# Optimization experiments

Measured on AMD Instinct MI355X. Metric: run time of the kernel, lower is better.

## Reference

```python
import jax, jax.numpy as jnp
import numpy as np

N, D_IN, D_HID, D_OUT, E = 8192, 1024, 4096, 1024, 8
N_ACTIVE = max(1, int(E * 0.625))  # 5
TEMP = float(np.e)               # temperature = np.e in source


def setup_inputs() -> dict:
    key = jax.random.key(0)
    ks = jax.random.split(key, 4)
    return {
        "x": jax.random.normal(ks[0], (N, D_IN), jnp.float32),
        "gate_w": jax.random.normal(ks[1], (D_IN, E), jnp.float32) * 0.02,
        "gate_b": jnp.zeros((E,), jnp.float32),
        "w1": jax.random.normal(ks[2], (E, D_IN, D_HID), jnp.float32) * 0.02,
        "b1": jnp.zeros((E, D_HID), jnp.float32),
        "w2": jax.random.normal(ks[3], (E, D_HID, D_OUT), jnp.float32) * 0.02,
        "b2": jnp.zeros((E, D_OUT), jnp.float32),
    }


def reference(x, gate_w, gate_b, w1, b1, w2, b2):
    # Gate: softmax over experts at temperature e, then top-k mask + renormalize
    scores = (x @ gate_w + gate_b) / TEMP                 # [N, E]
    probs = jax.nn.softmax(scores, axis=-1)               # [N, E]
    _, topk_idx = jax.lax.top_k(probs, N_ACTIVE)          # [N, k]
    mask = jax.nn.one_hot(topk_idx, E, dtype=probs.dtype).sum(axis=-2)  # [N, E]
    weights = probs * mask
    weights = weights / (weights.sum(axis=-1, keepdims=True) + 1e-8)
    # Dense all-experts FFN (dropout is eval-mode identity)
    h = jax.nn.relu(jnp.einsum('nd,edh->neh', x, w1) + b1)   # [N, E, d_hid]
    e_out = jnp.einsum('neh,eho->neo', h, w2) + b2           # [N, E, d_out]
    # Camp A (first E/2 experts) added, camp G subtracted: out = out_a - out_g
    sign = jnp.where(jnp.arange(E) < E // 2, 1.0, -1.0)      # [E]
    return jnp.einsum('ne,neo->no', weights * sign, e_out)   # [N, d_out]
```

## Files before the change

kernel.cpp:

```cpp
#include <hip/hip_runtime.h>
#include <hip/hip_bf16.h>
#include <cmath>


typedef _Float16 f16;
typedef _Float16 f16x8 __attribute__((ext_vector_type(8)));
typedef _Float16 f16x4 __attribute__((ext_vector_type(4)));
typedef float f32x4 __attribute__((ext_vector_type(4)));

#define NROWS 8192
#define DIN   1024
#define DHID  4096
#define DOUT  1024
#define NEXP  8

#define OFF_SGATE 0u
#define OFF_XH    262144u
#define OFF_W1T   17039360u
#define OFF_W2T   84148224u
#define OFF_HHS   151257088u
#define OFF_P1    218365952u
#define NEED_MID  251920384ull

__device__ __forceinline__ void gload_lds16(const void* gsrc, void* ldsdst) {
  __builtin_amdgcn_global_load_lds(
      (const __attribute__((address_space(1))) unsigned int*)gsrc,
      (__attribute__((address_space(3))) unsigned int*)ldsdst, 16, 0, 0);
}

__global__ void gate_kernel(const float* __restrict__ x,
                            const float* __restrict__ gw,
                            const float* __restrict__ gb,
                            float* __restrict__ sgate) {
  const int row = blockIdx.x * 4 + (threadIdx.x >> 6);
  const int l = threadIdx.x & 63;
  const float* xr = x + (size_t)row * DIN;
  float acc[8] = {0.f,0.f,0.f,0.f,0.f,0.f,0.f,0.f};
#pragma unroll
  for (int j = 0; j < 16; ++j) {
    const int k = l + 64 * j;
    const float xv = xr[k];
    const float4 g0 = *(const float4*)(gw + (size_t)k * 8);
    const float4 g1 = *(const float4*)(gw + (size_t)k * 8 + 4);
    acc[0] += xv * g0.x; acc[1] += xv * g0.y; acc[2] += xv * g0.z; acc[3] += xv * g0.w;
    acc[4] += xv * g1.x; acc[5] += xv * g1.y; acc[6] += xv * g1.z; acc[7] += xv * g1.w;
  }
#pragma unroll
  for (int off = 32; off > 0; off >>= 1) {
#pragma unroll
    for (int e = 0; e < 8; ++e) acc[e] += __shfl_xor(acc[e], off, 64);
  }
  if (l == 0) {
    const float invT = 0.36787944117144233f;
    float p[8]; float mx = -1e30f;
#pragma unroll
    for (int e = 0; e < 8; ++e) { p[e] = (acc[e] + gb[e]) * invT; mx = fmaxf(mx, p[e]); }
    float S = 0.f;
#pragma unroll
    for (int e = 0; e < 8; ++e) { p[e] = expf(p[e] - mx); S += p[e]; }
    const float inv = 1.0f / S;
#pragma unroll
    for (int e = 0; e < 8; ++e) p[e] *= inv;
    bool keep[8] = {true,true,true,true,true,true,true,true};
    for (int t = 0; t < 3; ++t) {
      float pmin = 1e30f; int mi = -1;
      for (int e = 0; e < 8; ++e)
        if (keep[e] && (p[e] < pmin || (p[e] == pmin && e > mi))) { pmin = p[e]; mi = e; }
      keep[mi] = false;
    }
    float wsum = 0.f;
#pragma unroll
    for (int e = 0; e < 8; ++e) if (keep[e]) wsum += p[e];
    const float rinv = 1.0f / (wsum + 1e-8f);
#pragma unroll
    for (int e = 0; e < 8; ++e) {
      const float wv = keep[e] ? p[e] * rinv : 0.0f;
      sgate[(size_t)row * 8 + e] = (e < 4) ? wv : -wv;
    }
  }
}

__global__ void cvt_x_kernel(const float* __restrict__ x, f16* __restrict__ xh) {
  const size_t i = ((size_t)blockIdx.x * blockDim.x + threadIdx.x) * 4;
  const float4 v = *(const float4*)(x + i);
  f16x4 o = { (f16)v.x, (f16)v.y, (f16)v.z, (f16)v.w };
  *(f16x4*)(xh + i) = o;
}

__global__ void transpose_cvt(const float* __restrict__ in, f16* __restrict__ out,
                              int R, int C) {
  __shared__ float tile[32][33];
  const int e = blockIdx.z;
  const float* ine = in + (size_t)e * R * C;
  f16* oute = out + (size_t)e * R * C;
  const int c0 = blockIdx.x * 32, r0 = blockIdx.y * 32;
  const int tx = threadIdx.x, ty = threadIdx.y;
#pragma unroll
  for (int i = 0; i < 4; ++i)
    tile[ty + i * 8][tx] = ine[(size_t)(r0 + ty + i * 8) * C + c0 + tx];
  __syncthreads();
#pragma unroll
  for (int i = 0; i < 4; ++i)
    oute[(size_t)(c0 + ty + i * 8) * R + r0 + tx] = (f16)tile[tx][ty + i * 8];
}

#define MFMAOP(a_, b_, c_) __builtin_amdgcn_mfma_f32_16x16x32_f16(a_, b_, c_, 0, 0, 0)

template <int EPI>
__global__ __launch_bounds__(512, 2) void gemm8p(
    const f16* __restrict__ A, int lda,
    const f16* __restrict__ B, int ldb, int nt,
    const float* __restrict__ bias,
    f16* __restrict__ outH, int ldc,
    float* outP0, float* outP1, int p1w,
    const float* __restrict__ sgate, int expert, int gx) {
  __shared__ alignas(16) f16 lA[4 * 8192];
  __shared__ alignas(16) f16 lB[4 * 8192];
  const int tid = threadIdx.x;
  const int l = tid & 63, w = tid >> 6;
  const int wr = w >> 2, wc = w & 3;

  const int nwg = gridDim.x, cpx = nwg >> 3;
  const int lg = ((int)blockIdx.x & 7) * cpx + ((int)blockIdx.x >> 3);

  int m0, n0;
  const f16* Aeff = A;
  const f16* Beff = B;
  float* P = nullptr;
  bool pw = false;
  if constexpr (EPI == 1) {
    m0 = (lg / gx) * 256; n0 = (lg % gx) * 256;
  } else {
    const int kh = lg & 1;
    const int tt = lg >> 1;
    m0 = (tt / gx) * 256; n0 = (tt % gx) * 256;
    Aeff = A + kh * 2048;
    Beff = B + kh * 2048;
    P = kh ? outP1 : outP0;
    pw = (p1w != 0);
  }

  const int srow = tid >> 3;
  const int sxc = (tid & 7) ^ (srow & 7);
  const f16* pA = Aeff + (size_t)(m0 + srow) * lda + sxc * 8;
  const f16* pB = Beff + (size_t)(n0 + srow) * ldb + sxc * 8;
  f16* const dA = lA + w * 512;
  f16* const dB = lB + w * 512;

#define STG_A(slot, h, tk) do { \
    const f16* s_ = pA + (size_t)(h) * 128 * lda + (size_t)(tk) * 64; \
    gload_lds16(s_,            dA + (slot) * 8192); \
    gload_lds16(s_ + 64 * lda, dA + (slot) * 8192 + 4096); \
  } while (0)
#define STG_B(slot, h, tk) do { \
    const f16* s_ = pB + (size_t)(h) * 128 * ldb + (size_t)(tk) * 64; \
    gload_lds16(s_,            dB + (slot) * 8192); \
    gload_lds16(s_ + 64 * ldb, dB + (slot) * 8192 + 4096); \
  } while (0)

  const int cg = l >> 4, xr = l & 7;
  const int ok0 = ((cg ^ xr) << 4);
  const int ok1 = (((4 + cg) ^ xr) << 4);
  const char* const baA = (const char*)lA + (l & 15) * 128;
  const char* const baB = (const char*)lB + (wc & 1) * 8192 + (l & 15) * 128;

#define RDA(CA, f, o) (*(const f16x8*)(baA + ((CA) + wr) * 16384 + (f) * 2048 + (o)))
#define RDB(CB, g, o) (*(const f16x8*)(baB + ((CB) + (wc >> 1)) * 16384 + (g) * 2048 + (o)))
#define SYNC() do { __builtin_amdgcn_s_barrier(); \
    asm volatile("s_waitcnt lgkmcnt(0)" ::: "memory"); \
    __builtin_amdgcn_sched_barrier(0); } while (0)
#define ENDPH() do { __builtin_amdgcn_s_setprio(0); \
    __builtin_amdgcn_s_barrier(); } while (0)
#define VM6() do { asm volatile("s_waitcnt vmcnt(6)" ::: "memory"); \
    __builtin_amdgcn_sched_barrier(0); } while (0)
#define MM(f, g, ar, br) acc[f][g] = MFMAOP(ar, br, acc[f][g])

  f32x4 acc[8][4] = {};
  f16x8 aA0,aA1,aB0,aB1,aC0,aC1,aD0,aD1;
  f16x8 b00,b01,b10,b11,b20,b21,b30,b31;

#define TILEBODY(T, CA, CB, SB1, SB0n, SA0n, SA1n) do { \
     \
    aA0 = RDA(CA, 0, ok0); aA1 = RDA(CA, 0, ok1); \
    aB0 = RDA(CA, 1, ok0); aB1 = RDA(CA, 1, ok1); \
    aC0 = RDA(CA, 2, ok0); aC1 = RDA(CA, 2, ok1); \
    aD0 = RDA(CA, 3, ok0); aD1 = RDA(CA, 3, ok1); \
    b00 = RDB(CB, 0, ok0); b01 = RDB(CB, 0, ok1); \
    b10 = RDB(CB, 1, ok0); b11 = RDB(CB, 1, ok1); \
    if ((T) + 1 < nt) STG_B(SB1, 1, (T) + 1); \
    SYNC(); \
    __builtin_amdgcn_s_setprio(1); \
    MM(0,0,aA0,b00); MM(0,1,aA0,b10); MM(1,0,aB0,b00); MM(1,1,aB0,b10); \
    MM(2,0,aC0,b00); MM(2,1,aC0,b10); MM(3,0,aD0,b00); MM(3,1,aD0,b10); \
    MM(0,0,aA1,b01); MM(0,1,aA1,b11); MM(1,0,aB1,b01); MM(1,1,aB1,b11); \
    MM(2,0,aC1,b01); MM(2,1,aC1,b11); MM(3,0,aD1,b01); MM(3,1,aD1,b11); \
    ENDPH(); \
     \
    b20 = RDB(CB, 2, ok0); b21 = RDB(CB, 2, ok1); \
    b30 = RDB(CB, 3, ok0); b31 = RDB(CB, 3, ok1); \
    SYNC(); \
    __builtin_amdgcn_s_setprio(1); \
    MM(0,2,aA0,b20); MM(0,3,aA0,b30); MM(1,2,aB0,b20); MM(1,3,aB0,b30); \
    MM(2,2,aC0,b20); MM(2,3,aC0,b30); MM(3,2,aD0,b20); MM(3,3,aD0,b30); \
    MM(0,2,aA1,b21); MM(0,3,aA1,b31); MM(1,2,aB1,b21); MM(1,3,aB1,b31); \
    MM(2,2,aC1,b21); MM(2,3,aC1,b31); MM(3,2,aD1,b21); MM(3,3,aD1,b31); \
    ENDPH(); \
     \
    aA0 = RDA(CA, 4, ok0); aA1 = RDA(CA, 4, ok1); \
    aB0 = RDA(CA, 5, ok0); aB1 = RDA(CA, 5, ok1); \
    aC0 = RDA(CA, 6, ok0); aC1 = RDA(CA, 6, ok1); \
    aD0 = RDA(CA, 7, ok0); aD1 = RDA(CA, 7, ok1); \
    if ((T) + 2 < nt) STG_B(SB0n, 0, (T) + 2); \
    SYNC(); \
    __builtin_amdgcn_s_setprio(1); \
    MM(4,0,aA0,b00); MM(4,1,aA0,b10); MM(5,0,aB0,b00); MM(5,1,aB0,b10); \
    MM(6,0,aC0,b00); MM(6,1,aC0,b10); MM(7,0,aD0,b00); MM(7,1,aD0,b10); \
    MM(4,0,aA1,b01); MM(4,1,aA1,b11); MM(5,0,aB1,b01); MM(5,1,aB1,b11); \
    MM(6,0,aC1,b01); MM(6,1,aC1,b11); MM(7,0,aD1,b01); MM(7,1,aD1,b11); \
    ENDPH(); \
     \
    if ((T) + 2 < nt) { STG_A(SA0n, 0, (T) + 2); STG_A(SA1n, 1, (T) + 2); } \
    VM6(); \
    SYNC(); \
    __builtin_amdgcn_s_setprio(1); \
    MM(4,2,aA0,b20); MM(4,3,aA0,b30); MM(5,2,aB0,b20); MM(5,3,aB0,b30); \
    MM(6,2,aC0,b20); MM(6,3,aC0,b30); MM(7,2,aD0,b20); MM(7,3,aD0,b30); \
    MM(4,2,aA1,b21); MM(4,3,aA1,b31); MM(5,2,aB1,b21); MM(5,3,aB1,b31); \
    MM(6,2,aC1,b21); MM(6,3,aC1,b31); MM(7,2,aD1,b21); MM(7,3,aD1,b31); \
    ENDPH(); \
  } while (0)

  STG_A(0, 0, 0); STG_B(0, 0, 0); STG_A(1, 1, 0); STG_B(1, 1, 0);
  STG_A(2, 0, 1); STG_B(2, 0, 1); STG_A(3, 1, 1);
  asm volatile("s_waitcnt vmcnt(6)" ::: "memory");
  __builtin_amdgcn_s_barrier();

  for (int t = 0; t < nt; t += 2) {
    TILEBODY(t,     0, 0, 3, 0, 0, 1);
    TILEBODY(t + 1, 2, 2, 1, 2, 2, 3);
  }
  asm volatile("s_waitcnt vmcnt(0)" ::: "memory");

  if constexpr (EPI == 1) {
#pragma unroll
    for (int mi = 0; mi < 8; ++mi)
#pragma unroll
      for (int r = 0; r < 4; ++r) {
        const int row = m0 + wr * 128 + mi * 16 + (l >> 4) * 4 + r;
        const float sg = sgate[(size_t)row * 8 + expert];
#pragma unroll
        for (int ni = 0; ni < 4; ++ni) {
          const int col = n0 + wc * 64 + ni * 16 + (l & 15);
          const float v = acc[mi][ni][r] + bias[col];
          outH[(size_t)row * ldc + col] = (f16)(fmaxf(v, 0.0f) * sg);
        }
      }
  } else {
#pragma unroll
    for (int mi = 0; mi < 8; ++mi)
#pragma unroll
      for (int r = 0; r < 4; ++r) {
        const int row = m0 + wr * 128 + mi * 16 + (l >> 4) * 4 + r;
#pragma unroll
        for (int ni = 0; ni < 4; ++ni) {
          const int col = n0 + wc * 64 + ni * 16 + (l & 15);
          const size_t ix = (size_t)row * 1024 + col;
          float v = acc[mi][ni][r];
          if (!pw) v += P[ix];
          P[ix] = v;
        }
      }
  }
#undef STG_A
#undef STG_B
#undef RDA
#undef RDB
#undef SYNC
#undef ENDPH
#undef VM6
#undef MM
#undef TILEBODY
}

template <bool WITHP>
__global__ void finalize_out(const float* p0,
                             const float* __restrict__ p1,
                             const float* __restrict__ sgate,
                             const float* __restrict__ b2,
                             float* out) {
  const int i = blockIdx.x * 256 + threadIdx.x;
  const int n = i >> 8, c4 = i & 255;
  float4 a = make_float4(0.f, 0.f, 0.f, 0.f);
  if constexpr (WITHP) {
    const float4 u = ((const float4*)p0)[i];
    const float4 v = ((const float4*)p1)[i];
    a.x = u.x + v.x; a.y = u.y + v.y; a.z = u.z + v.z; a.w = u.w + v.w;
  }
  const float* sg = sgate + (size_t)n * 8;
#pragma unroll
  for (int e = 0; e < 8; ++e) {
    const float s = sg[e];
    const float4 bv = ((const float4*)(b2 + (size_t)e * 1024))[c4];
    a.x += s * bv.x; a.y += s * bv.y; a.z += s * bv.z; a.w += s * bv.w;
  }
  ((float4*)out)[i] = a;
}

__global__ __launch_bounds__(512, 2) void gemm_acc(
    const f16* __restrict__ A, const f16* __restrict__ Bt,
    float* __restrict__ Out, int N, int K, int gx) {
  __shared__ alignas(16) f16 lA[3 * 256 * 64];
  __shared__ alignas(16) f16 lB[3 * 128 * 64];
  const int tid = threadIdx.x;
  const int l = tid & 63, w = tid >> 6;
  const int wr = w >> 1, wc = w & 1;
  const int nwg = gridDim.x, cpx = nwg >> 3;
  const int lg = ((int)blockIdx.x & 7) * cpx + ((int)blockIdx.x >> 3);
  const int bx = lg % gx, by = lg / gx;
  const int m0 = by * 256, n0 = bx * 128;

  const int srow = tid >> 3;
  const int scol = (((tid & 7) ^ (srow & 7)) << 3);
  const f16* Ab = A + ((size_t)m0 + srow) * K + scol;
  const f16* Bb = Bt + ((size_t)n0 + srow) * K + scol;
  f16* const dA = &lA[w * 512];
  f16* const dB = &lB[w * 512];

  int aoff[4][2], boff[4][2];
#pragma unroll
  for (int f = 0; f < 4; ++f) {
    const int ar = wr * 64 + f * 16 + (l & 15);
    const int br = wc * 64 + f * 16 + (l & 15);
#pragma unroll
    for (int ks = 0; ks < 2; ++ks) {
      const int cb = ks * 64 + ((l >> 4) << 4);
      aoff[f][ks] = ar * 64 + ((cb ^ ((ar & 7) << 4)) >> 1);
      boff[f][ks] = br * 64 + ((cb ^ ((br & 7) << 4)) >> 1);
    }
  }
  f32x4 acc[4][4] = {};
  f16x8 b[4][2];
  f16x8 aA, aB, aC, aD;
#define STAGE_A(bs, t) do { \
    const f16* s_ = Ab + (size_t)(t) * 64; \
    gload_lds16(s_,                   dA + (bs) * 16384); \
    gload_lds16(s_ + (size_t)64 * K,  dA + (bs) * 16384 + 4096); \
    gload_lds16(s_ + (size_t)128 * K, dA + (bs) * 16384 + 8192); \
    gload_lds16(s_ + (size_t)192 * K, dA + (bs) * 16384 + 12288); \
  } while (0)
#define STAGE_B(bs, t) do { \
    const f16* s_ = Bb + (size_t)(t) * 64; \
    gload_lds16(s_,                   dB + (bs) * 8192); \
    gload_lds16(s_ + (size_t)64 * K,  dB + (bs) * 8192 + 4096); \
  } while (0)
#define LOAD_B(bs) do { \
    b[0][0] = *(const f16x8*)&lB[(bs) * 8192 + boff[0][0]]; \
    b[0][1] = *(const f16x8*)&lB[(bs) * 8192 + boff[0][1]]; \
    b[1][0] = *(const f16x8*)&lB[(bs) * 8192 + boff[1][0]]; \
    b[1][1] = *(const f16x8*)&lB[(bs) * 8192 + boff[1][1]]; \
    b[2][0] = *(const f16x8*)&lB[(bs) * 8192 + boff[2][0]]; \
    b[2][1] = *(const f16x8*)&lB[(bs) * 8192 + boff[2][1]]; \
    b[3][0] = *(const f16x8*)&lB[(bs) * 8192 + boff[3][0]]; \
    b[3][1] = *(const f16x8*)&lB[(bs) * 8192 + boff[3][1]]; \
  } while (0)
#define LOAD_A4(bs, m0_, m1_) do { \
    aA = *(const f16x8*)&lA[(bs) * 16384 + aoff[m0_][0]]; \
    aB = *(const f16x8*)&lA[(bs) * 16384 + aoff[m0_][1]]; \
    aC = *(const f16x8*)&lA[(bs) * 16384 + aoff[m1_][0]]; \
    aD = *(const f16x8*)&lA[(bs) * 16384 + aoff[m1_][1]]; \
  } while (0)
#define CLUSTER(m0_, m1_) do { \
    __builtin_amdgcn_s_setprio(1); \
    acc[m0_][0] = MFMAOP(aA, b[0][0], acc[m0_][0]); \
    acc[m0_][1] = MFMAOP(aA, b[1][0], acc[m0_][1]); \
    acc[m0_][2] = MFMAOP(aA, b[2][0], acc[m0_][2]); \
    acc[m0_][3] = MFMAOP(aA, b[3][0], acc[m0_][3]); \
    acc[m1_][0] = MFMAOP(aC, b[0][0], acc[m1_][0]); \
    acc[m1_][1] = MFMAOP(aC, b[1][0], acc[m1_][1]); \
    acc[m1_][2] = MFMAOP(aC, b[2][0], acc[m1_][2]); \
    acc[m1_][3] = MFMAOP(aC, b[3][0], acc[m1_][3]); \
    acc[m0_][0] = MFMAOP(aB, b[0][1], acc[m0_][0]); \
    acc[m0_][1] = MFMAOP(aB, b[1][1], acc[m0_][1]); \
    acc[m0_][2] = MFMAOP(aB, b[2][1], acc[m0_][2]); \
    acc[m0_][3] = MFMAOP(aB, b[3][1], acc[m0_][3]); \
    acc[m1_][0] = MFMAOP(aD, b[0][1], acc[m1_][0]); \
    acc[m1_][1] = MFMAOP(aD, b[1][1], acc[m1_][1]); \
    acc[m1_][2] = MFMAOP(aD, b[2][1], acc[m1_][2]); \
    acc[m1_][3] = MFMAOP(aD, b[3][1], acc[m1_][3]); \
    __builtin_amdgcn_s_setprio(0); \
  } while (0)
#define BAR() asm volatile("s_barrier" ::: "memory")
#define VMC6() asm volatile("s_waitcnt vmcnt(6)" ::: "memory")
  const int niter = K >> 7, ntiles = K >> 6;
  STAGE_A(0, 0); STAGE_B(0, 0);
  STAGE_A(1, 1); STAGE_B(1, 1);
  VMC6();
  BAR();
  int bp = 0, bq = 1, brr = 2;
  int t2 = 2, t3 = 3;
  for (int i = 0; i < niter; ++i) {
    LOAD_B(bp); LOAD_A4(bp, 0, 1);
    STAGE_A(brr, t2);
    BAR(); CLUSTER(0, 1); BAR();
    LOAD_A4(bp, 2, 3);
    STAGE_B(brr, t2);
    VMC6(); BAR(); CLUSTER(2, 3); BAR();
    LOAD_B(bq); LOAD_A4(bq, 0, 1);
    STAGE_A(bp, t3);
    BAR(); CLUSTER(0, 1); BAR();
    LOAD_A4(bq, 2, 3);
    STAGE_B(bp, t3);
    VMC6(); BAR(); CLUSTER(2, 3); BAR();
    const int tmp = bp; bp = brr; brr = bq; bq = tmp;
    t2 += 2; if (t2 >= ntiles) t2 -= ntiles;
    t3 += 2; if (t3 >= ntiles) t3 -= ntiles;
  }
  asm volatile("s_waitcnt vmcnt(0)" ::: "memory");
#pragma unroll
  for (int mi = 0; mi < 4; ++mi)
#pragma unroll
    for (int r = 0; r < 4; ++r) {
      const int row = m0 + wr * 64 + mi * 16 + (l >> 4) * 4 + r;
#pragma unroll
      for (int ni = 0; ni < 4; ++ni) {
        const int col = n0 + wc * 64 + ni * 16 + (l & 15);
        Out[(size_t)row * N + col] += acc[mi][ni][r];
      }
    }
#undef STAGE_A
#undef STAGE_B
#undef LOAD_B
#undef LOAD_A4
#undef CLUSTER
#undef BAR
#undef VMC6
}

extern "C" void kernel_launch(void* const* d_in, const int* in_sizes, int n_in,
                              void* d_out, int out_size, void* d_ws, size_t ws_size,
                              hipStream_t stream) {
  const float* x  = (const float*)d_in[0];
  const float* gw = (const float*)d_in[1];
  const float* gb = (const float*)d_in[2];
  const float* w1 = (const float*)d_in[3];
  const float* b1 = (const float*)d_in[4];
  const float* w2 = (const float*)d_in[5];
  const float* b2 = (const float*)d_in[6];
  float* out = (float*)d_out;

  char* ws = (char*)d_ws;
  float* sgate = (float*)(ws + OFF_SGATE);
  f16* xh  = (f16*)(ws + OFF_XH);
  f16* w1t = (f16*)(ws + OFF_W1T);
  f16* w2t = (f16*)(ws + OFF_W2T);
  f16* hhs = (f16*)(ws + OFF_HHS);
  float* p1 = (float*)(ws + OFF_P1);

  const bool mid = (ws_size >= NEED_MID);

  gate_kernel<<<NROWS / 4, 256, 0, stream>>>(x, gw, gb, sgate);
  cvt_x_kernel<<<(NROWS * DIN) / (256 * 4), 256, 0, stream>>>(x, xh);
  transpose_cvt<<<dim3(DHID / 32, DIN / 32, NEXP), dim3(32, 8), 0, stream>>>(w1, w1t, DIN, DHID);
  transpose_cvt<<<dim3(DOUT / 32, DHID / 32, NEXP), dim3(32, 8), 0, stream>>>(w2, w2t, DHID, DOUT);

  if (mid) {
    for (int e = 0; e < NEXP; ++e) {
      gemm8p<1><<<512, 512, 0, stream>>>(
          xh, DIN, w1t + (size_t)e * DHID * DIN, DIN, DIN / 64,
          b1 + (size_t)e * DHID, hhs, DHID,
          nullptr, nullptr, 0, sgate, e, DHID / 256);
      gemm8p<2><<<256, 512, 0, stream>>>(
          hhs, DHID, w2t + (size_t)e * DOUT * DHID, DHID, 2048 / 64,
          nullptr, nullptr, 0, out, p1, (e == 0) ? 1 : 0, nullptr, 0, DOUT / 256);
    }
    finalize_out<true><<<(NROWS * DOUT) / (256 * 4), 256, 0, stream>>>(
        out, p1, sgate, b2, out);
  } else {
    finalize_out<false><<<(NROWS * DOUT) / (256 * 4), 256, 0, stream>>>(
        nullptr, nullptr, sgate, b2, out);
    for (int e = 0; e < NEXP; ++e) {
      gemm8p<1><<<512, 512, 0, stream>>>(
          xh, DIN, w1t + (size_t)e * DHID * DIN, DIN, DIN / 64,
          b1 + (size_t)e * DHID, hhs, DHID,
          nullptr, nullptr, 0, sgate, e, DHID / 256);
      gemm_acc<<<256, 512, 0, stream>>>(hhs, w2t + (size_t)e * DOUT * DHID,
                                        out, DOUT, DHID, DOUT / 128);
    }
  }
}
```

Baseline: 1.504 ms.

## Vectorize GEMM2 partial-sum epilogue via LDS transpose and remap tile order

The second-GEMM epilogue now stages each wave's accumulator tile through LDS scratch, reusing the A/B buffers, and then does 16-byte vector read-modify-writes of the fp32 partial buffers instead of scalar strided accesses. The block-to-tile mapping for the split-K GEMM is also changed so that consecutive block groups walk along M with fixed N and K-half. This targets the cost of uncoalesced scalar global traffic in the epilogue and aims for better L2 locality. It adds LDS round trips and relies on the main loop having finished with LDS, since no barrier is added before the scratch writes.

```diff
diff --git a/kernel.cpp b/kernel.cpp
--- a/kernel.cpp
+++ b/kernel.cpp
@@ -131,9 +131,10 @@
   if constexpr (EPI == 1) {
     m0 = (lg / gx) * 256; n0 = (lg % gx) * 256;
   } else {
-    const int kh = lg & 1;
-    const int tt = lg >> 1;
-    m0 = (tt / gx) * 256; n0 = (tt % gx) * 256;
+    const int xx = lg >> 5, cc = lg & 31;
+    const int kh = xx >> 2;
+    n0 = (xx & 3) * 256;
+    m0 = cc * 256;
     Aeff = A + kh * 2048;
     Beff = B + kh * 2048;
     P = kh ? outP1 : outP0;
@@ -256,20 +257,34 @@
         }
       }
   } else {
-#pragma unroll
-    for (int mi = 0; mi < 8; ++mi)
-#pragma unroll
-      for (int r = 0; r < 4; ++r) {
-        const int row = m0 + wr * 128 + mi * 16 + (l >> 4) * 4 + r;
-#pragma unroll
-        for (int ni = 0; ni < 4; ++ni) {
-          const int col = n0 + wc * 64 + ni * 16 + (l & 15);
-          const size_t ix = (size_t)row * 1024 + col;
-          float v = acc[mi][ni][r];
-          if (!pw) v += P[ix];
-          P[ix] = v;
+    float* const scr = (w < 4) ? (float*)lA + w * 4096
+                               : (float*)lB + (w - 4) * 4096;
+    const int hl = l >> 4, ll = l & 15;
+#pragma unroll
+    for (int p = 0; p < 2; ++p) {
+#pragma unroll
+      for (int mi4 = 0; mi4 < 4; ++mi4)
+#pragma unroll
+        for (int r = 0; r < 4; ++r) {
+          const int rowl = mi4 * 16 + hl * 4 + r;
+#pragma unroll
+          for (int ni = 0; ni < 4; ++ni)
+            scr[rowl * 64 + ni * 16 + ll] = acc[p * 4 + mi4][ni][r];
         }
+#pragma unroll
+      for (int i = 0; i < 16; ++i) {
+        const int rowl = hl + i * 4;
+        f32x4 v = *(const f32x4*)(scr + rowl * 64 + ll * 4);
+        const int row = m0 + wr * 128 + p * 64 + rowl;
+        const int col = n0 + wc * 64 + ll * 4;
+        f32x4* gp = (f32x4*)(P + (size_t)row * 1024 + col);
+        if (!pw) {
+          const f32x4 g = *gp;
+          v[0] += g[0]; v[1] += g[1]; v[2] += g[2]; v[3] += g[3];
+        }
+        *gp = v;
       }
+    }
   }
 #undef STG_A
 #undef STG_B
```

Result: slower. 1.545 ms (+2.8%).
